# Performance work log

Measured on AMD Instinct MI355X. Metric: run time of the kernel, lower is better.

## Reference

```python
import jax, jax.numpy as jnp
import numpy as np

B, T, D = 1024, 64, 512
HID = 256          # hamiltonian_field hidden width
NH = 4             # attention heads
HD = D // NH       # head dim


def _gelu(x):
    # torch nn.GELU default = exact erf form
    return jax.nn.gelu(x, approximate=False)


def _field(z, W1, b1, W2, b2, W3, b3):
    h = _gelu(z @ W1.T + b1)
    h = _gelu(h @ W2.T + b2)
    return h @ W3.T + b3


def setup_inputs() -> dict:
    key = jax.random.key(0)
    ks = jax.random.split(key, 14)
    s = 0.02  # small-gain init like orthogonal_(gain=0.02)
    f32 = jnp.float32
    return {
        "z_init": jax.random.normal(ks[0], (B, D), f32),
        "t_steps": jnp.arange(T, dtype=f32) * 0.05,  # dt = 0.05
        "W1": jax.random.normal(ks[1], (HID, D), f32) * s,
        "b1": jnp.zeros((HID,), f32),
        "W2": jax.random.normal(ks[2], (HID, HID), f32) * s,
        "b2": jnp.zeros((HID,), f32),
        "W3": jax.random.normal(ks[3], (D, HID), f32) * s,
        "b3": jnp.zeros((D,), f32),
        "Wqkv": jax.random.normal(ks[4], (3 * D, D), f32) * (1.0 / np.sqrt(D)),
        "bqkv": jnp.zeros((3 * D,), f32),
        "Wo": jax.random.normal(ks[5], (D, D), f32) * (1.0 / np.sqrt(D)),
        "bo": jnp.zeros((D,), f32),
        "gamma": jnp.ones((D,), f32),
        "beta": jnp.zeros((D,), f32),
    }


def _forward(z_init, t_steps, W1, b1, W2, b2, W3, b3, Wqkv, bqkv, Wo, bo, gamma, beta):
    dt = t_steps[1] - t_steps[0]
    # input-adaptive scale, computed under no_grad in torch
    zn = jnp.linalg.norm(z_init, axis=-1, keepdims=True)
    zv = jnp.var(z_init, axis=-1, ddof=1, keepdims=True)  # torch.var unbiased
    scale = jax.lax.stop_gradient(jnp.clip(zn / (zv + 1e-6), 0.8, 1.2))
    z0 = z_init * scale

    f = lambda z: _field(z, W1, b1, W2, b2, W3, b3)

    def rk4_step(zt, _):
        k1 = f(zt)
        k2 = f(zt + dt * 0.5 * k1)
        k3 = f(zt + dt * 0.5 * k2)
        k4 = f(zt + dt * k3)
        z_new = zt + dt / 6.0 * (k1 + 2.0 * k2 + 2.0 * k3 + k4)
        z_new = jnp.where(jnp.isnan(z_new), 0.0, z_new)
        return z_new, z_new

    _, outs = jax.lax.scan(rk4_step, z0, None, length=T)  # [T,B,D]
    z_stack = jnp.transpose(outs, (1, 0, 2))              # [B,T,D]

    z_mean = jnp.mean(z_stack, axis=1, keepdims=True)
    z_dc = z_stack - 0.05 * (z_mean - z_init[:, None, :])

    # (torch code also computes rfft magnitudes / argmax here, but the result
    # is unused in the returned output, so it is omitted.)

    # multi-head self-attention, batch_first
    qkv = z_dc @ Wqkv.T + bqkv                            # [B,T,3D]
    q, k, v = jnp.split(qkv, 3, axis=-1)
    q = q.reshape(B, T, NH, HD)
    k = k.reshape(B, T, NH, HD)
    v = v.reshape(B, T, NH, HD)
    scores = jnp.einsum("bqhd,bkhd->bhqk", q, k) / jnp.sqrt(jnp.float32(HD))
    att = jax.nn.softmax(scores, axis=-1)
    ctx = jnp.einsum("bhqk,bkhd->bqhd", att, v).reshape(B, T, D)
    att_out = ctx @ Wo.T + bo

    # residual + LayerNorm (eps=1e-5)
    x = z_dc + att_out
    mu = jnp.mean(x, axis=-1, keepdims=True)
    var = jnp.var(x, axis=-1, keepdims=True)
    z_final = (x - mu) / jnp.sqrt(var + 1e-5) * gamma + beta
    z_final = jnp.where(jnp.isnan(z_final), 0.0, z_final)
    return z_final


def reference(z_init, t_steps, W1, b1, W2, b2, W3, b3, Wqkv, bqkv, Wo, bo, gamma, beta):
    return _forward(z_init, t_steps, W1, b1, W2, b2, W3, b3, Wqkv, bqkv, Wo, bo, gamma, beta)
```

## Files before the change

### kernel.cpp

```cpp
#include <hip/hip_runtime.h>

typedef short s16;
typedef short bf16x8 __attribute__((ext_vector_type(8)));
typedef float f32x4 __attribute__((ext_vector_type(4)));

constexpr int kB = 1024, kT = 64, kD = 512, kH = 256;
constexpr int NSEG = 14;
constexpr int kOff[NSEG] = {0, 524288, 524352, 655424, 655680, 721216, 721472,
                            852544, 853056, 1639488, 1641024, 1903168, 1903680, 1904192};
constexpr int kTotalConv = 1904704;

__device__ __forceinline__ float bs2f(s16 s) {
    return __uint_as_float(((unsigned)(unsigned short)s) << 16);
}
__device__ __forceinline__ s16 f2bs(float f) {
    unsigned u = __float_as_uint(f);
    unsigned r = (u + 0x7fffu + ((u >> 16) & 1u)) >> 16;
    return (s16)r;
}
__device__ __forceinline__ f32x4 mfma16(bf16x8 a, bf16x8 b, f32x4 c) {
    return __builtin_amdgcn_mfma_f32_16x16x32_bf16(a, b, c, 0, 0, 0);
}
__device__ __forceinline__ float gelu(float x) {
    return 0.5f * x * (1.0f + erff(x * 0.70710678118654752f));
}

__global__ void detect_kernel(const unsigned* __restrict__ ts, int* __restrict__ flag) {
    if (threadIdx.x == 0 && blockIdx.x == 0) flag[0] = (ts[0] == 0u) ? 1 : 0;
}

struct ConvArgs { const void* src[NSEG]; };

__global__ __launch_bounds__(256) void convert_kernel(ConvArgs a, s16* __restrict__ dst,
                                                      const int* __restrict__ flag) {
    const int f = flag[0];
    for (int i = blockIdx.x * 256 + threadIdx.x; i < kTotalConv; i += gridDim.x * 256) {
        int s = 0;
        #pragma unroll
        for (int j = 1; j < NSEG; ++j) if (i >= kOff[j]) s = j;
        int local = i - kOff[s];
        s16 v;
        if (f) v = f2bs(((const float*)a.src[s])[local]);
        else   v = ((const s16*)a.src[s])[local];
        dst[i] = v;
    }
}

__global__ __launch_bounds__(512, 2) void ode_kernel(
    const s16* __restrict__ zin, const s16* __restrict__ ts,
    const s16* __restrict__ W1, const s16* __restrict__ b1,
    const s16* __restrict__ W2, const s16* __restrict__ b2,
    const s16* __restrict__ W3, const s16* __restrict__ b3,
    s16* __restrict__ stage)
{
    __shared__ __align__(16) s16 sArg[16 * 520];
    __shared__ __align__(16) s16 sH1[16 * 264];
    __shared__ __align__(16) s16 sH2[16 * 264];
    __shared__ float sScale[16];

    const int tid = threadIdx.x;
    const int w = tid >> 6;
    const int lane = tid & 63;
    const int quad = lane >> 4;
    const int c = lane & 15;
    const int r0 = blockIdx.x * 16;

    const float dt  = bs2f(ts[1]) - bs2f(ts[0]);
    const float hdt = 0.5f * dt;
    const float dt6 = dt / 6.0f;

    for (int r = w; r < 16; r += 8) {
        const s16* zrow = zin + (size_t)(r0 + r) * kD;
        float sum = 0.f, ssq = 0.f;
        for (int i = 0; i < 8; ++i) {
            float v = bs2f(zrow[lane + 64 * i]);
            sum += v; ssq += v * v;
        }
        for (int m = 1; m < 64; m <<= 1) {
            sum += __shfl_xor(sum, m, 64);
            ssq += __shfl_xor(ssq, m, 64);
        }
        float zn = sqrtf(ssq);
        float mean = sum / (float)kD;
        float var = (ssq - (float)kD * mean * mean) / (float)(kD - 1);
        float sc = zn / (var + 1e-6f);
        sc = fminf(fmaxf(sc, 0.8f), 1.2f);
        if (lane == 0) sScale[r] = sc;
    }

    bf16x8 w2r[2][8];
    #pragma unroll
    for (int nt = 0; nt < 2; ++nt)
        #pragma unroll
        for (int kk = 0; kk < 8; ++kk)
            w2r[nt][kk] = *(const bf16x8*)(W2 + (size_t)(w * 32 + nt * 16 + c) * kH + kk * 32 + quad * 8);

    __syncthreads();

    const int colbase = w * 64;
    float zreg[4][4], accR[4][4];
    #pragma unroll
    for (int nt = 0; nt < 4; ++nt)
        #pragma unroll
        for (int rr = 0; rr < 4; ++rr) {
            int m = quad * 4 + rr, col = colbase + nt * 16 + c;
            zreg[nt][rr] = bs2f(zin[(size_t)(r0 + m) * kD + col]) * sScale[m];
            accR[nt][rr] = 0.f;
        }
    for (int r = w; r < 16; r += 8) {
        const s16* zrow = zin + (size_t)(r0 + r) * kD;
        float sc = sScale[r];
        s16* dst = sArg + r * 520 + lane * 8;
        #pragma unroll
        for (int j = 0; j < 8; ++j) dst[j] = f2bs(bs2f(zrow[lane * 8 + j]) * sc);
    }
    float b1v[2], b2v[2], b3v[4];
    #pragma unroll
    for (int nt = 0; nt < 2; ++nt) {
        b1v[nt] = bs2f(b1[w * 32 + nt * 16 + c]);
        b2v[nt] = bs2f(b2[w * 32 + nt * 16 + c]);
    }
    #pragma unroll
    for (int nt = 0; nt < 4; ++nt) b3v[nt] = bs2f(b3[colbase + nt * 16 + c]);

    const int w1o = (w * 32 + c) * kD + quad * 8;
    const int w3o = (w * 64 + c) * kH + quad * 8;

    __syncthreads();

    #pragma unroll 1
    for (int t = 0; t < kT; ++t) {
        #pragma unroll 1
        for (int e = 0; e < 4; ++e) {
            int ow1 = w1o, ow3 = w3o;
            asm volatile("" : "+v"(ow1), "+v"(ow3));
            const s16* W1p = W1 + ow1;
            const s16* W3p = W3 + ow3;

            f32x4 a1[2];
            a1[0] = {0.f, 0.f, 0.f, 0.f};
            a1[1] = {0.f, 0.f, 0.f, 0.f};
            #pragma unroll
            for (int kk = 0; kk < 16; ++kk) {
                bf16x8 av = *(const bf16x8*)(sArg + c * 520 + kk * 32 + quad * 8);
                bf16x8 b0 = *(const bf16x8*)(W1p + kk * 32);
                bf16x8 b1f = *(const bf16x8*)(W1p + 16 * kD + kk * 32);
                a1[0] = mfma16(av, b0, a1[0]);
                a1[1] = mfma16(av, b1f, a1[1]);
            }
            #pragma unroll
            for (int nt = 0; nt < 2; ++nt)
                #pragma unroll
                for (int rr = 0; rr < 4; ++rr)
                    sH1[(quad * 4 + rr) * 264 + w * 32 + nt * 16 + c] = f2bs(gelu(a1[nt][rr] + b1v[nt]));
            __syncthreads();

            f32x4 a2[2];
            a2[0] = {0.f, 0.f, 0.f, 0.f};
            a2[1] = {0.f, 0.f, 0.f, 0.f};
            #pragma unroll
            for (int kk = 0; kk < 8; ++kk) {
                bf16x8 av = *(const bf16x8*)(sH1 + c * 264 + kk * 32 + quad * 8);
                a2[0] = mfma16(av, w2r[0][kk], a2[0]);
                a2[1] = mfma16(av, w2r[1][kk], a2[1]);
            }
            #pragma unroll
            for (int nt = 0; nt < 2; ++nt)
                #pragma unroll
                for (int rr = 0; rr < 4; ++rr)
                    sH2[(quad * 4 + rr) * 264 + w * 32 + nt * 16 + c] = f2bs(gelu(a2[nt][rr] + b2v[nt]));
            __syncthreads();

            f32x4 a3[4];
            #pragma unroll
            for (int nt = 0; nt < 4; ++nt) a3[nt] = {0.f, 0.f, 0.f, 0.f};
            #pragma unroll
            for (int kk = 0; kk < 8; ++kk) {
                bf16x8 av = *(const bf16x8*)(sH2 + c * 264 + kk * 32 + quad * 8);
                #pragma unroll
                for (int nt = 0; nt < 4; ++nt) {
                    bf16x8 bb = *(const bf16x8*)(W3p + nt * 16 * kH + kk * 32);
                    a3[nt] = mfma16(av, bb, a3[nt]);
                }
            }
            const float wsum = (e == 0 || e == 3) ? 1.f : 2.f;
            const float cstep = (e == 2) ? dt : hdt;
            #pragma unroll
            for (int nt = 0; nt < 4; ++nt) {
                #pragma unroll
                for (int rr = 0; rr < 4; ++rr) {
                    float fv = a3[nt][rr] + b3v[nt];
                    accR[nt][rr] += wsum * fv;
                    int m = quad * 4 + rr;
                    int col = colbase + nt * 16 + c;
                    float argv;
                    if (e < 3) {
                        argv = zreg[nt][rr] + cstep * fv;
                    } else {
                        float zn2 = zreg[nt][rr] + dt6 * accR[nt][rr];
                        zn2 = (zn2 != zn2) ? 0.f : zn2;
                        zreg[nt][rr] = zn2;
                        accR[nt][rr] = 0.f;
                        argv = zn2;
                        stage[(size_t)(r0 + m) * kT * kD + (size_t)t * kD + col] = f2bs(zn2);
                    }
                    sArg[m * 520 + col] = f2bs(argv);
                }
            }
            __syncthreads();
        }
    }
}

__global__ __launch_bounds__(256) void attn_kernel(
    const s16* __restrict__ zin,
    const s16* __restrict__ Wqkv, const s16* __restrict__ bqkv,
    const s16* __restrict__ Wo, const s16* __restrict__ bo,
    const s16* __restrict__ gm, const s16* __restrict__ bt,
    const s16* __restrict__ stage, void* __restrict__ outp,
    const int* __restrict__ flag, int mode)
{
    __shared__ __align__(16) s16 sQ[64 * 136];
    __shared__ __align__(16) s16 sK[64 * 136];
    __shared__ __align__(16) s16 sVT[128 * 72];
    __shared__ __align__(16) s16 sMean[512];
    __shared__ __align__(16) s16 sZi[512];
    float* psum = (float*)sQ;

    const int tid = threadIdx.x;
    const int w = tid >> 6, lane = tid & 63, quad = lane >> 4, c = lane & 15;
    const int b = blockIdx.x;
    const int f32out = mode ? flag[0] : 0;
    const s16* zs = stage + (size_t)b * kT * kD;

    for (int i = tid; i < kD; i += 256) sZi[i] = zin[(size_t)b * kD + i];
    {
        float s[8] = {0, 0, 0, 0, 0, 0, 0, 0};
        const int phase = tid >> 6, cg = (tid & 63) * 8;
        for (int i = 0; i < 16; ++i) {
            int t = phase + 4 * i;
            bf16x8 v = *(const bf16x8*)(zs + (size_t)t * kD + cg);
            #pragma unroll
            for (int j = 0; j < 8; ++j) s[j] += bs2f(v[j]);
        }
        #pragma unroll
        for (int j = 0; j < 8; ++j) psum[phase * kD + cg + j] = s[j];
    }
    __syncthreads();
    for (int col = tid; col < kD; col += 256) {
        float m = (psum[col] + psum[kD + col] + psum[2 * kD + col] + psum[3 * kD + col]) * (1.f / 64.f);
        sMean[col] = f2bs(m);
    }
    __syncthreads();

    bf16x8 afrag[16];
    #pragma unroll
    for (int kk = 0; kk < 16; ++kk) {
        int k0 = kk * 32 + quad * 8;
        bf16x8 zv = *(const bf16x8*)(zs + (size_t)(w * 16 + c) * kD + k0);
        bf16x8 o;
        #pragma unroll
        for (int j = 0; j < 8; ++j) {
            float zd = bs2f(zv[j]) - 0.05f * (bs2f(sMean[k0 + j]) - bs2f(sZi[k0 + j]));
            o[j] = f2bs(zd);
        }
        afrag[kk] = o;
    }

    f32x4 xacc[32];
    #pragma unroll
    for (int nt = 0; nt < 32; ++nt) xacc[nt] = {0.f, 0.f, 0.f, 0.f};

    const float iscl = 0.08838834764831845f;

    for (int h = 0; h < 4; ++h) {
        __syncthreads();
        for (int mat = 0; mat < 3; ++mat) {
            f32x4 acc[8];
            #pragma unroll
            for (int nt = 0; nt < 8; ++nt) acc[nt] = {0.f, 0.f, 0.f, 0.f};
            const s16* Wbase = Wqkv + (size_t)(mat * 512 + h * 128 + c) * kD + quad * 8;
            #pragma unroll
            for (int kk = 0; kk < 16; ++kk) {
                bf16x8 a = afrag[kk];
                #pragma unroll
                for (int nt = 0; nt < 8; ++nt) {
                    bf16x8 bb = *(const bf16x8*)(Wbase + (size_t)(nt * 16) * kD + kk * 32);
                    acc[nt] = mfma16(a, bb, acc[nt]);
                }
            }
            #pragma unroll
            for (int nt = 0; nt < 8; ++nt)
                #pragma unroll
                for (int rr = 0; rr < 4; ++rr) {
                    int n = h * 128 + nt * 16 + c;
                    float v = acc[nt][rr] + bs2f(bqkv[mat * 512 + n]);
                    int trow = w * 16 + quad * 4 + rr, dcol = nt * 16 + c;
                    if (mat == 0)      sQ[trow * 136 + dcol] = f2bs(v);
                    else if (mat == 1) sK[trow * 136 + dcol] = f2bs(v);
                    else               sVT[dcol * 72 + trow] = f2bs(v);
                }
        }
        __syncthreads();

        f32x4 sfr[4];
        #pragma unroll
        for (int nt = 0; nt < 4; ++nt) sfr[nt] = {0.f, 0.f, 0.f, 0.f};
        #pragma unroll
        for (int kk = 0; kk < 4; ++kk) {
            bf16x8 a = *(const bf16x8*)(sQ + (w * 16 + c) * 136 + kk * 32 + quad * 8);
            #pragma unroll
            for (int nt = 0; nt < 4; ++nt) {
                bf16x8 bb = *(const bf16x8*)(sK + (nt * 16 + c) * 136 + kk * 32 + quad * 8);
                sfr[nt] = mfma16(a, bb, sfr[nt]);
            }
        }
        #pragma unroll
        for (int rr = 0; rr < 4; ++rr) {
            float v[4];
            #pragma unroll
            for (int nt = 0; nt < 4; ++nt) v[nt] = sfr[nt][rr] * iscl;
            float mx = fmaxf(fmaxf(v[0], v[1]), fmaxf(v[2], v[3]));
            for (int m = 1; m < 16; m <<= 1) mx = fmaxf(mx, __shfl_xor(mx, m, 64));
            float sm = 0.f;
            #pragma unroll
            for (int nt = 0; nt < 4; ++nt) { v[nt] = __expf(v[nt] - mx); sm += v[nt]; }
            for (int m = 1; m < 16; m <<= 1) sm += __shfl_xor(sm, m, 64);
            float inv = 1.0f / sm;
            #pragma unroll
            for (int nt = 0; nt < 4; ++nt)
                sQ[(w * 16 + quad * 4 + rr) * 136 + nt * 16 + c] = f2bs(v[nt] * inv);
        }
        f32x4 o[8];
        #pragma unroll
        for (int nt = 0; nt < 8; ++nt) o[nt] = {0.f, 0.f, 0.f, 0.f};
        #pragma unroll
        for (int kk = 0; kk < 2; ++kk) {
            bf16x8 a = *(const bf16x8*)(sQ + (w * 16 + c) * 136 + kk * 32 + quad * 8);
            #pragma unroll
            for (int nt = 0; nt < 8; ++nt) {
                bf16x8 bb = *(const bf16x8*)(sVT + (nt * 16 + c) * 72 + kk * 32 + quad * 8);
                o[nt] = mfma16(a, bb, o[nt]);
            }
        }
        #pragma unroll
        for (int nt = 0; nt < 8; ++nt)
            #pragma unroll
            for (int rr = 0; rr < 4; ++rr)
                sQ[(w * 16 + quad * 4 + rr) * 136 + nt * 16 + c] = f2bs(o[nt][rr]);
        #pragma unroll
        for (int kk = 0; kk < 4; ++kk) {
            bf16x8 a = *(const bf16x8*)(sQ + (w * 16 + c) * 136 + kk * 32 + quad * 8);
            #pragma unroll
            for (int nt = 0; nt < 32; ++nt) {
                bf16x8 bb = *(const bf16x8*)(Wo + (size_t)(nt * 16 + c) * kD + h * 128 + kk * 32 + quad * 8);
                xacc[nt] = mfma16(a, bb, xacc[nt]);
            }
        }
    }

    float sum[4] = {0, 0, 0, 0}, ssq[4] = {0, 0, 0, 0};
    #pragma unroll
    for (int nt = 0; nt < 32; ++nt)
        #pragma unroll
        for (int rr = 0; rr < 4; ++rr) {
            int trow = w * 16 + quad * 4 + rr;
            int col = nt * 16 + c;
            float zd = bs2f(zs[(size_t)trow * kD + col]) - 0.05f * (bs2f(sMean[col]) - bs2f(sZi[col]));
            float x = xacc[nt][rr] + bs2f(bo[col]) + zd;
            xacc[nt][rr] = x;
            sum[rr] += x; ssq[rr] += x * x;
        }
    float mu[4], rstd[4];
    #pragma unroll
    for (int rr = 0; rr < 4; ++rr) {
        float s = sum[rr], q = ssq[rr];
        for (int m = 1; m < 16; m <<= 1) { s += __shfl_xor(s, m, 64); q += __shfl_xor(q, m, 64); }
        float mm = s / (float)kD;
        float var = q / (float)kD - mm * mm;
        mu[rr] = mm;
        rstd[rr] = rsqrtf(var + 1e-5f);
    }
    #pragma unroll
    for (int nt = 0; nt < 32; ++nt)
        #pragma unroll
        for (int rr = 0; rr < 4; ++rr) {
            int trow = w * 16 + quad * 4 + rr;
            int col = nt * 16 + c;
            float v = (xacc[nt][rr] - mu[rr]) * rstd[rr] * bs2f(gm[col]) + bs2f(bt[col]);
            v = (v != v) ? 0.f : v;
            size_t idx = ((size_t)b * kT + trow) * kD + col;
            if (f32out) ((float*)outp)[idx] = v;
            else        ((s16*)outp)[idx] = f2bs(v);
        }
}

extern "C" void kernel_launch(void* const* d_in, const int* in_sizes, int n_in,
                              void* d_out, int out_size, void* d_ws, size_t ws_size,
                              hipStream_t stream) {
    (void)in_sizes; (void)n_in; (void)out_size;
    const size_t kStageElems = (size_t)kB * kT * kD;
    const size_t kNeed = 16 + (size_t)kTotalConv * 2 + kStageElems * 2;

    const s16* p[NSEG];
    s16* stage;
    void* outp = d_out;
    const int* flag = nullptr;
    int mode = 0;

    if (ws_size >= kNeed) {
        int* flg = (int*)d_ws;
        s16* conv = (s16*)((char*)d_ws + 16);
        stage = (s16*)((char*)d_ws + 16 + (size_t)kTotalConv * 2);
        detect_kernel<<<dim3(1), dim3(64), 0, stream>>>((const unsigned*)d_in[1], flg);
        ConvArgs ca;
        for (int i = 0; i < NSEG; ++i) ca.src[i] = d_in[i];
        convert_kernel<<<dim3(512), dim3(256), 0, stream>>>(ca, conv, flg);
        for (int i = 0; i < NSEG; ++i) p[i] = conv + kOff[i];
        flag = flg;
        mode = 1;
    } else {
        for (int i = 0; i < NSEG; ++i) p[i] = (const s16*)d_in[i];
        stage = (s16*)d_out;
    }

    ode_kernel<<<dim3(64), dim3(512), 0, stream>>>(
        p[0], p[1], p[2], p[3], p[4], p[5], p[6], p[7], stage);
    attn_kernel<<<dim3(kB), dim3(256), 0, stream>>>(
        p[0], p[8], p[9], p[10], p[11], p[12], p[13], stage, outp, flag, mode);
}
```

Before: 6.275 ms.

## Batch weight loads with inline-asm dwordx4 and prefetch W3 during layer two

Replaces compiler-scheduled W1/W3 global loads inside the RK4 field evaluation with explicit inline-asm global_load_dwordx4 batches of 16 registers, each followed by a single vmcnt(0) wait. The W3 loads for the first half of layer 3 are issued before the layer-2 MFMAs and the barrier, so their latency can overlap that work. The goal is to hide global or L2 load latency that previously stalled the MFMA chains. In exchange the kernel holds more live VGPRs for the staged weights, and the blanket vmcnt(0) waits may over-serialize.

```diff
diff --git a/kernel.cpp b/kernel.cpp
--- a/kernel.cpp
+++ b/kernel.cpp
@@ -24,6 +24,11 @@
 __device__ __forceinline__ float gelu(float x) {
     return 0.5f * x * (1.0f + erff(x * 0.70710678118654752f));
 }
+
+#define GLD(dst, ptr, OFF) \
+    asm volatile("global_load_dwordx4 %0, %1, off offset:" #OFF : "=v"(dst) : "v"(ptr))
+#define VMWAIT0 do { asm volatile("s_waitcnt vmcnt(0)" ::: "memory"); \
+                     __builtin_amdgcn_sched_barrier(0); } while (0)
 
 __global__ void detect_kernel(const unsigned* __restrict__ ts, int* __restrict__ flag) {
     if (threadIdx.x == 0 && blockIdx.x == 0) flag[0] = (ts[0] == 0u) ? 1 : 0;
@@ -87,14 +92,6 @@
         sc = fminf(fmaxf(sc, 0.8f), 1.2f);
         if (lane == 0) sScale[r] = sc;
     }
-
-    bf16x8 w2r[2][8];
-    #pragma unroll
-    for (int nt = 0; nt < 2; ++nt)
-        #pragma unroll
-        for (int kk = 0; kk < 8; ++kk)
-            w2r[nt][kk] = *(const bf16x8*)(W2 + (size_t)(w * 32 + nt * 16 + c) * kH + kk * 32 + quad * 8);
-
     __syncthreads();
 
     const int colbase = w * 64;
@@ -123,8 +120,25 @@
     #pragma unroll
     for (int nt = 0; nt < 4; ++nt) b3v[nt] = bs2f(b3[colbase + nt * 16 + c]);
 
-    const int w1o = (w * 32 + c) * kD + quad * 8;
-    const int w3o = (w * 64 + c) * kH + quad * 8;
+    const s16* w1p0 = W1 + (size_t)(w * 32 + c) * kD + quad * 8;
+    const s16* w1p1 = w1p0 + 16 * kD;
+    const s16* w2p0 = W2 + (size_t)(w * 32 + c) * kH + quad * 8;
+    const s16* w2p1 = w2p0 + 16 * kH;
+    const s16* w3p0 = W3 + (size_t)(w * 64 + c) * kH + quad * 8;
+    const s16* w3p1 = w3p0 + 16 * kH;
+    const s16* w3p2 = w3p0 + 32 * kH;
+    const s16* w3p3 = w3p0 + 48 * kH;
+
+    bf16x8 w2r[16];
+    GLD(w2r[0],  w2p0, 0);   GLD(w2r[1],  w2p1, 0);
+    GLD(w2r[2],  w2p0, 64);  GLD(w2r[3],  w2p1, 64);
+    GLD(w2r[4],  w2p0, 128); GLD(w2r[5],  w2p1, 128);
+    GLD(w2r[6],  w2p0, 192); GLD(w2r[7],  w2p1, 192);
+    GLD(w2r[8],  w2p0, 256); GLD(w2r[9],  w2p1, 256);
+    GLD(w2r[10], w2p0, 320); GLD(w2r[11], w2p1, 320);
+    GLD(w2r[12], w2p0, 384); GLD(w2r[13], w2p1, 384);
+    GLD(w2r[14], w2p0, 448); GLD(w2r[15], w2p1, 448);
+    VMWAIT0;
 
     __syncthreads();
 
@@ -132,57 +146,105 @@
     for (int t = 0; t < kT; ++t) {
         #pragma unroll 1
         for (int e = 0; e < 4; ++e) {
-            int ow1 = w1o, ow3 = w3o;
-            asm volatile("" : "+v"(ow1), "+v"(ow3));
-            const s16* W1p = W1 + ow1;
-            const s16* W3p = W3 + ow3;
-
-            f32x4 a1[2];
-            a1[0] = {0.f, 0.f, 0.f, 0.f};
-            a1[1] = {0.f, 0.f, 0.f, 0.f};
-            #pragma unroll
-            for (int kk = 0; kk < 16; ++kk) {
-                bf16x8 av = *(const bf16x8*)(sArg + c * 520 + kk * 32 + quad * 8);
-                bf16x8 b0 = *(const bf16x8*)(W1p + kk * 32);
-                bf16x8 b1f = *(const bf16x8*)(W1p + 16 * kD + kk * 32);
-                a1[0] = mfma16(av, b0, a1[0]);
-                a1[1] = mfma16(av, b1f, a1[1]);
-            }
-            #pragma unroll
-            for (int nt = 0; nt < 2; ++nt)
-                #pragma unroll
-                for (int rr = 0; rr < 4; ++rr)
-                    sH1[(quad * 4 + rr) * 264 + w * 32 + nt * 16 + c] = f2bs(gelu(a1[nt][rr] + b1v[nt]));
+            f32x4 a1n0 = {0.f, 0.f, 0.f, 0.f}, a1n1 = {0.f, 0.f, 0.f, 0.f};
+            {
+                bf16x8 wf[16];
+                GLD(wf[0],  w1p0, 0);   GLD(wf[1],  w1p1, 0);
+                GLD(wf[2],  w1p0, 64);  GLD(wf[3],  w1p1, 64);
+                GLD(wf[4],  w1p0, 128); GLD(wf[5],  w1p1, 128);
+                GLD(wf[6],  w1p0, 192); GLD(wf[7],  w1p1, 192);
+                GLD(wf[8],  w1p0, 256); GLD(wf[9],  w1p1, 256);
+                GLD(wf[10], w1p0, 320); GLD(wf[11], w1p1, 320);
+                GLD(wf[12], w1p0, 384); GLD(wf[13], w1p1, 384);
+                GLD(wf[14], w1p0, 448); GLD(wf[15], w1p1, 448);
+                VMWAIT0;
+                #pragma unroll
+                for (int kk = 0; kk < 8; ++kk) {
+                    bf16x8 av = *(const bf16x8*)(sArg + c * 520 + kk * 32 + quad * 8);
+                    a1n0 = mfma16(av, wf[kk * 2 + 0], a1n0);
+                    a1n1 = mfma16(av, wf[kk * 2 + 1], a1n1);
+                }
+                GLD(wf[0],  w1p0, 512); GLD(wf[1],  w1p1, 512);
+                GLD(wf[2],  w1p0, 576); GLD(wf[3],  w1p1, 576);
+                GLD(wf[4],  w1p0, 640); GLD(wf[5],  w1p1, 640);
+                GLD(wf[6],  w1p0, 704); GLD(wf[7],  w1p1, 704);
+                GLD(wf[8],  w1p0, 768); GLD(wf[9],  w1p1, 768);
+                GLD(wf[10], w1p0, 832); GLD(wf[11], w1p1, 832);
+                GLD(wf[12], w1p0, 896); GLD(wf[13], w1p1, 896);
+                GLD(wf[14], w1p0, 960); GLD(wf[15], w1p1, 960);
+                VMWAIT0;
+                #pragma unroll
+                for (int kk = 0; kk < 8; ++kk) {
+                    bf16x8 av = *(const bf16x8*)(sArg + c * 520 + (8 + kk) * 32 + quad * 8);
+                    a1n0 = mfma16(av, wf[kk * 2 + 0], a1n0);
+                    a1n1 = mfma16(av, wf[kk * 2 + 1], a1n1);
+                }
+            }
+            sH1[(quad * 4 + 0) * 264 + w * 32 + 0 * 16 + c] = f2bs(gelu(a1n0[0] + b1v[0]));
+            sH1[(quad * 4 + 1) * 264 + w * 32 + 0 * 16 + c] = f2bs(gelu(a1n0[1] + b1v[0]));
+            sH1[(quad * 4 + 2) * 264 + w * 32 + 0 * 16 + c] = f2bs(gelu(a1n0[2] + b1v[0]));
+            sH1[(quad * 4 + 3) * 264 + w * 32 + 0 * 16 + c] = f2bs(gelu(a1n0[3] + b1v[0]));
+            sH1[(quad * 4 + 0) * 264 + w * 32 + 1 * 16 + c] = f2bs(gelu(a1n1[0] + b1v[1]));
+            sH1[(quad * 4 + 1) * 264 + w * 32 + 1 * 16 + c] = f2bs(gelu(a1n1[1] + b1v[1]));
+            sH1[(quad * 4 + 2) * 264 + w * 32 + 1 * 16 + c] = f2bs(gelu(a1n1[2] + b1v[1]));
+            sH1[(quad * 4 + 3) * 264 + w * 32 + 1 * 16 + c] = f2bs(gelu(a1n1[3] + b1v[1]));
             __syncthreads();
 
-            f32x4 a2[2];
-            a2[0] = {0.f, 0.f, 0.f, 0.f};
-            a2[1] = {0.f, 0.f, 0.f, 0.f};
+            bf16x8 w3x[16];
+            GLD(w3x[0],  w3p0, 0);   GLD(w3x[1],  w3p1, 0);
+            GLD(w3x[2],  w3p2, 0);   GLD(w3x[3],  w3p3, 0);
+            GLD(w3x[4],  w3p0, 64);  GLD(w3x[5],  w3p1, 64);
+            GLD(w3x[6],  w3p2, 64);  GLD(w3x[7],  w3p3, 64);
+            GLD(w3x[8],  w3p0, 128); GLD(w3x[9],  w3p1, 128);
+            GLD(w3x[10], w3p2, 128); GLD(w3x[11], w3p3, 128);
+            GLD(w3x[12], w3p0, 192); GLD(w3x[13], w3p1, 192);
+            GLD(w3x[14], w3p2, 192); GLD(w3x[15], w3p3, 192);
+
+            f32x4 a2n0 = {0.f, 0.f, 0.f, 0.f}, a2n1 = {0.f, 0.f, 0.f, 0.f};
             #pragma unroll
             for (int kk = 0; kk < 8; ++kk) {
                 bf16x8 av = *(const bf16x8*)(sH1 + c * 264 + kk * 32 + quad * 8);
-                a2[0] = mfma16(av, w2r[0][kk], a2[0]);
-                a2[1] = mfma16(av, w2r[1][kk], a2[1]);
-            }
-            #pragma unroll
-            for (int nt = 0; nt < 2; ++nt)
-                #pragma unroll
-                for (int rr = 0; rr < 4; ++rr)
-                    sH2[(quad * 4 + rr) * 264 + w * 32 + nt * 16 + c] = f2bs(gelu(a2[nt][rr] + b2v[nt]));
+                a2n0 = mfma16(av, w2r[kk * 2 + 0], a2n0);
+                a2n1 = mfma16(av, w2r[kk * 2 + 1], a2n1);
+            }
+            sH2[(quad * 4 + 0) * 264 + w * 32 + 0 * 16 + c] = f2bs(gelu(a2n0[0] + b2v[0]));
+            sH2[(quad * 4 + 1) * 264 + w * 32 + 0 * 16 + c] = f2bs(gelu(a2n0[1] + b2v[0]));
+            sH2[(quad * 4 + 2) * 264 + w * 32 + 0 * 16 + c] = f2bs(gelu(a2n0[2] + b2v[0]));
+            sH2[(quad * 4 + 3) * 264 + w * 32 + 0 * 16 + c] = f2bs(gelu(a2n0[3] + b2v[0]));
+            sH2[(quad * 4 + 0) * 264 + w * 32 + 1 * 16 + c] = f2bs(gelu(a2n1[0] + b2v[1]));
+            sH2[(quad * 4 + 1) * 264 + w * 32 + 1 * 16 + c] = f2bs(gelu(a2n1[1] + b2v[1]));
+            sH2[(quad * 4 + 2) * 264 + w * 32 + 1 * 16 + c] = f2bs(gelu(a2n1[2] + b2v[1]));
+            sH2[(quad * 4 + 3) * 264 + w * 32 + 1 * 16 + c] = f2bs(gelu(a2n1[3] + b2v[1]));
             __syncthreads();
 
+            VMWAIT0;
             f32x4 a3[4];
             #pragma unroll
             for (int nt = 0; nt < 4; ++nt) a3[nt] = {0.f, 0.f, 0.f, 0.f};
             #pragma unroll
-            for (int kk = 0; kk < 8; ++kk) {
+            for (int kk = 0; kk < 4; ++kk) {
                 bf16x8 av = *(const bf16x8*)(sH2 + c * 264 + kk * 32 + quad * 8);
                 #pragma unroll
-                for (int nt = 0; nt < 4; ++nt) {
-                    bf16x8 bb = *(const bf16x8*)(W3p + nt * 16 * kH + kk * 32);
-                    a3[nt] = mfma16(av, bb, a3[nt]);
-                }
-            }
+                for (int nt = 0; nt < 4; ++nt)
+                    a3[nt] = mfma16(av, w3x[kk * 4 + nt], a3[nt]);
+            }
+            GLD(w3x[0],  w3p0, 256); GLD(w3x[1],  w3p1, 256);
+            GLD(w3x[2],  w3p2, 256); GLD(w3x[3],  w3p3, 256);
+            GLD(w3x[4],  w3p0, 320); GLD(w3x[5],  w3p1, 320);
+            GLD(w3x[6],  w3p2, 320); GLD(w3x[7],  w3p3, 320);
+            GLD(w3x[8],  w3p0, 384); GLD(w3x[9],  w3p1, 384);
+            GLD(w3x[10], w3p2, 384); GLD(w3x[11], w3p3, 384);
+            GLD(w3x[12], w3p0, 448); GLD(w3x[13], w3p1, 448);
+            GLD(w3x[14], w3p2, 448); GLD(w3x[15], w3p3, 448);
+            VMWAIT0;
+            #pragma unroll
+            for (int kk = 0; kk < 4; ++kk) {
+                bf16x8 av = *(const bf16x8*)(sH2 + c * 264 + (4 + kk) * 32 + quad * 8);
+                #pragma unroll
+                for (int nt = 0; nt < 4; ++nt)
+                    a3[nt] = mfma16(av, w3x[kk * 4 + nt], a3[nt]);
+            }
+
             const float wsum = (e == 0 || e == 3) ? 1.f : 2.f;
             const float cstep = (e == 2) ? dt : hdt;
             #pragma unroll
```

Measured after the change: 6.122 ms. 2.4% less time.

## Split ODE field work over 16 waves with hand-pipelined weight loads

Applied to the files above, without the earlier changes.

Doubles the ODE block to 1024 threads (16 waves), so each wave owns half as many output columns per layer. W2 is no longer held in registers and is reloaded every stage. W1, W2 and W3 fragments are now fetched with inline-asm dwordx4 loads issued ahead of use, with staged vmcnt waits so global latency overlaps the MFMA chains. Barriers become a raw lgkmcnt wait plus s_barrier. The aim is to hide the latency of the serial RK4 chain with more waves and explicit prefetch, at the cost of more weight traffic from L2 and fragile hand-counted waits.

```diff
diff --git a/kernel.cpp b/kernel.cpp
--- a/kernel.cpp
+++ b/kernel.cpp
@@ -24,6 +24,15 @@
 __device__ __forceinline__ float gelu(float x) {
     return 0.5f * x * (1.0f + erff(x * 0.70710678118654752f));
 }
+
+#define GLD(dst, ptr, OFF) \
+    asm volatile("global_load_dwordx4 %0, %1, off offset:" #OFF : "=v"(dst) : "v"(ptr))
+#define VMWAIT(N) do { asm volatile("s_waitcnt vmcnt(" #N ")" ::: "memory"); \
+                       __builtin_amdgcn_sched_barrier(0); } while (0)
+#define LDSBAR do { asm volatile("s_waitcnt lgkmcnt(0)" ::: "memory"); \
+                    __builtin_amdgcn_s_barrier(); \
+                    asm volatile("" ::: "memory"); \
+                    __builtin_amdgcn_sched_barrier(0); } while (0)
 
 __global__ void detect_kernel(const unsigned* __restrict__ ts, int* __restrict__ flag) {
     if (threadIdx.x == 0 && blockIdx.x == 0) flag[0] = (ts[0] == 0u) ? 1 : 0;
@@ -46,7 +55,7 @@
     }
 }
 
-__global__ __launch_bounds__(512, 2) void ode_kernel(
+__global__ __launch_bounds__(1024) void ode_kernel(
     const s16* __restrict__ zin, const s16* __restrict__ ts,
     const s16* __restrict__ W1, const s16* __restrict__ b1,
     const s16* __restrict__ W2, const s16* __restrict__ b2,
@@ -69,8 +78,8 @@
     const float hdt = 0.5f * dt;
     const float dt6 = dt / 6.0f;
 
-    for (int r = w; r < 16; r += 8) {
-        const s16* zrow = zin + (size_t)(r0 + r) * kD;
+    {
+        const s16* zrow = zin + (size_t)(r0 + w) * kD;
         float sum = 0.f, ssq = 0.f;
         for (int i = 0; i < 8; ++i) {
             float v = bs2f(zrow[lane + 64 * i]);
@@ -85,46 +94,37 @@
         float var = (ssq - (float)kD * mean * mean) / (float)(kD - 1);
         float sc = zn / (var + 1e-6f);
         sc = fminf(fmaxf(sc, 0.8f), 1.2f);
-        if (lane == 0) sScale[r] = sc;
-    }
-
-    bf16x8 w2r[2][8];
+        if (lane == 0) sScale[w] = sc;
+    }
+    __syncthreads();
+
+    const int colbase = w * 32;
+    float zreg[2][4], accR[2][4];
     #pragma unroll
     for (int nt = 0; nt < 2; ++nt)
-        #pragma unroll
-        for (int kk = 0; kk < 8; ++kk)
-            w2r[nt][kk] = *(const bf16x8*)(W2 + (size_t)(w * 32 + nt * 16 + c) * kH + kk * 32 + quad * 8);
-
-    __syncthreads();
-
-    const int colbase = w * 64;
-    float zreg[4][4], accR[4][4];
-    #pragma unroll
-    for (int nt = 0; nt < 4; ++nt)
         #pragma unroll
         for (int rr = 0; rr < 4; ++rr) {
             int m = quad * 4 + rr, col = colbase + nt * 16 + c;
             zreg[nt][rr] = bs2f(zin[(size_t)(r0 + m) * kD + col]) * sScale[m];
             accR[nt][rr] = 0.f;
         }
-    for (int r = w; r < 16; r += 8) {
-        const s16* zrow = zin + (size_t)(r0 + r) * kD;
-        float sc = sScale[r];
-        s16* dst = sArg + r * 520 + lane * 8;
+    {
+        const s16* zrow = zin + (size_t)(r0 + w) * kD;
+        float sc = sScale[w];
+        s16* dst = sArg + w * 520 + lane * 8;
         #pragma unroll
         for (int j = 0; j < 8; ++j) dst[j] = f2bs(bs2f(zrow[lane * 8 + j]) * sc);
     }
-    float b1v[2], b2v[2], b3v[4];
-    #pragma unroll
-    for (int nt = 0; nt < 2; ++nt) {
-        b1v[nt] = bs2f(b1[w * 32 + nt * 16 + c]);
-        b2v[nt] = bs2f(b2[w * 32 + nt * 16 + c]);
-    }
-    #pragma unroll
-    for (int nt = 0; nt < 4; ++nt) b3v[nt] = bs2f(b3[colbase + nt * 16 + c]);
-
-    const int w1o = (w * 32 + c) * kD + quad * 8;
-    const int w3o = (w * 64 + c) * kH + quad * 8;
+    const float b1v = bs2f(b1[w * 16 + c]);
+    const float b2v = bs2f(b2[w * 16 + c]);
+    float b3v[2];
+    b3v[0] = bs2f(b3[colbase + c]);
+    b3v[1] = bs2f(b3[colbase + 16 + c]);
+
+    const s16* w1p  = W1 + (size_t)(w * 16 + c) * kD + quad * 8;
+    const s16* w2p  = W2 + (size_t)(w * 16 + c) * kH + quad * 8;
+    const s16* w3p0 = W3 + (size_t)(w * 32 + c) * kH + quad * 8;
+    const s16* w3p1 = w3p0 + 16 * kH;
 
     __syncthreads();
 
@@ -132,61 +132,94 @@
     for (int t = 0; t < kT; ++t) {
         #pragma unroll 1
         for (int e = 0; e < 4; ++e) {
-            int ow1 = w1o, ow3 = w3o;
-            asm volatile("" : "+v"(ow1), "+v"(ow3));
-            const s16* W1p = W1 + ow1;
-            const s16* W3p = W3 + ow3;
-
-            f32x4 a1[2];
-            a1[0] = {0.f, 0.f, 0.f, 0.f};
-            a1[1] = {0.f, 0.f, 0.f, 0.f};
-            #pragma unroll
-            for (int kk = 0; kk < 16; ++kk) {
+            bf16x8 f1a[8], f1b[8], f2w[8];
+            GLD(f1a[0], w1p, 0);   GLD(f1a[1], w1p, 64);
+            GLD(f1a[2], w1p, 128); GLD(f1a[3], w1p, 192);
+            GLD(f1a[4], w1p, 256); GLD(f1a[5], w1p, 320);
+            GLD(f1a[6], w1p, 384); GLD(f1a[7], w1p, 448);
+            GLD(f1b[0], w1p, 512); GLD(f1b[1], w1p, 576);
+            GLD(f1b[2], w1p, 640); GLD(f1b[3], w1p, 704);
+            GLD(f1b[4], w1p, 768); GLD(f1b[5], w1p, 832);
+            GLD(f1b[6], w1p, 896); GLD(f1b[7], w1p, 960);
+            VMWAIT(8);
+            f32x4 a1 = {0.f, 0.f, 0.f, 0.f};
+            #pragma unroll
+            for (int kk = 0; kk < 8; ++kk) {
                 bf16x8 av = *(const bf16x8*)(sArg + c * 520 + kk * 32 + quad * 8);
-                bf16x8 b0 = *(const bf16x8*)(W1p + kk * 32);
-                bf16x8 b1f = *(const bf16x8*)(W1p + 16 * kD + kk * 32);
-                a1[0] = mfma16(av, b0, a1[0]);
-                a1[1] = mfma16(av, b1f, a1[1]);
-            }
-            #pragma unroll
-            for (int nt = 0; nt < 2; ++nt)
-                #pragma unroll
-                for (int rr = 0; rr < 4; ++rr)
-                    sH1[(quad * 4 + rr) * 264 + w * 32 + nt * 16 + c] = f2bs(gelu(a1[nt][rr] + b1v[nt]));
-            __syncthreads();
-
-            f32x4 a2[2];
-            a2[0] = {0.f, 0.f, 0.f, 0.f};
-            a2[1] = {0.f, 0.f, 0.f, 0.f};
+                a1 = mfma16(av, f1a[kk], a1);
+            }
+            GLD(f2w[0], w2p, 0);   GLD(f2w[1], w2p, 64);
+            GLD(f2w[2], w2p, 128); GLD(f2w[3], w2p, 192);
+            GLD(f2w[4], w2p, 256); GLD(f2w[5], w2p, 320);
+            GLD(f2w[6], w2p, 384); GLD(f2w[7], w2p, 448);
+            VMWAIT(8);
+            #pragma unroll
+            for (int kk = 0; kk < 8; ++kk) {
+                bf16x8 av = *(const bf16x8*)(sArg + c * 520 + (8 + kk) * 32 + quad * 8);
+                a1 = mfma16(av, f1b[kk], a1);
+            }
+            #pragma unroll
+            for (int rr = 0; rr < 4; ++rr)
+                sH1[(quad * 4 + rr) * 264 + w * 16 + c] = f2bs(gelu(a1[rr] + b1v));
+            LDSBAR;
+
+            bf16x8 f3a[4], f3b[4], f3c[4], f3d[4];
+            GLD(f3a[0], w3p0, 0);   GLD(f3a[1], w3p1, 0);
+            GLD(f3a[2], w3p0, 64);  GLD(f3a[3], w3p1, 64);
+            GLD(f3b[0], w3p0, 128); GLD(f3b[1], w3p1, 128);
+            GLD(f3b[2], w3p0, 192); GLD(f3b[3], w3p1, 192);
+            VMWAIT(8);
+            f32x4 a2 = {0.f, 0.f, 0.f, 0.f};
             #pragma unroll
             for (int kk = 0; kk < 8; ++kk) {
                 bf16x8 av = *(const bf16x8*)(sH1 + c * 264 + kk * 32 + quad * 8);
-                a2[0] = mfma16(av, w2r[0][kk], a2[0]);
-                a2[1] = mfma16(av, w2r[1][kk], a2[1]);
-            }
-            #pragma unroll
-            for (int nt = 0; nt < 2; ++nt)
-                #pragma unroll
-                for (int rr = 0; rr < 4; ++rr)
-                    sH2[(quad * 4 + rr) * 264 + w * 32 + nt * 16 + c] = f2bs(gelu(a2[nt][rr] + b2v[nt]));
-            __syncthreads();
-
-            f32x4 a3[4];
-            #pragma unroll
-            for (int nt = 0; nt < 4; ++nt) a3[nt] = {0.f, 0.f, 0.f, 0.f};
-            #pragma unroll
-            for (int kk = 0; kk < 8; ++kk) {
+                a2 = mfma16(av, f2w[kk], a2);
+            }
+            GLD(f3c[0], w3p0, 256); GLD(f3c[1], w3p1, 256);
+            GLD(f3c[2], w3p0, 320); GLD(f3c[3], w3p1, 320);
+            GLD(f3d[0], w3p0, 384); GLD(f3d[1], w3p1, 384);
+            GLD(f3d[2], w3p0, 448); GLD(f3d[3], w3p1, 448);
+            #pragma unroll
+            for (int rr = 0; rr < 4; ++rr)
+                sH2[(quad * 4 + rr) * 264 + w * 16 + c] = f2bs(gelu(a2[rr] + b2v));
+            LDSBAR;
+
+            f32x4 a3[2];
+            a3[0] = {0.f, 0.f, 0.f, 0.f};
+            a3[1] = {0.f, 0.f, 0.f, 0.f};
+            VMWAIT(12);
+            #pragma unroll
+            for (int kk = 0; kk < 2; ++kk) {
                 bf16x8 av = *(const bf16x8*)(sH2 + c * 264 + kk * 32 + quad * 8);
-                #pragma unroll
-                for (int nt = 0; nt < 4; ++nt) {
-                    bf16x8 bb = *(const bf16x8*)(W3p + nt * 16 * kH + kk * 32);
-                    a3[nt] = mfma16(av, bb, a3[nt]);
-                }
-            }
+                a3[0] = mfma16(av, f3a[kk * 2 + 0], a3[0]);
+                a3[1] = mfma16(av, f3a[kk * 2 + 1], a3[1]);
+            }
+            VMWAIT(8);
+            #pragma unroll
+            for (int kk = 2; kk < 4; ++kk) {
+                bf16x8 av = *(const bf16x8*)(sH2 + c * 264 + kk * 32 + quad * 8);
+                a3[0] = mfma16(av, f3b[(kk - 2) * 2 + 0], a3[0]);
+                a3[1] = mfma16(av, f3b[(kk - 2) * 2 + 1], a3[1]);
+            }
+            VMWAIT(4);
+            #pragma unroll
+            for (int kk = 4; kk < 6; ++kk) {
+                bf16x8 av = *(const bf16x8*)(sH2 + c * 264 + kk * 32 + quad * 8);
+                a3[0] = mfma16(av, f3c[(kk - 4) * 2 + 0], a3[0]);
+                a3[1] = mfma16(av, f3c[(kk - 4) * 2 + 1], a3[1]);
+            }
+            VMWAIT(0);
+            #pragma unroll
+            for (int kk = 6; kk < 8; ++kk) {
+                bf16x8 av = *(const bf16x8*)(sH2 + c * 264 + kk * 32 + quad * 8);
+                a3[0] = mfma16(av, f3d[(kk - 6) * 2 + 0], a3[0]);
+                a3[1] = mfma16(av, f3d[(kk - 6) * 2 + 1], a3[1]);
+            }
+
             const float wsum = (e == 0 || e == 3) ? 1.f : 2.f;
             const float cstep = (e == 2) ? dt : hdt;
             #pragma unroll
-            for (int nt = 0; nt < 4; ++nt) {
+            for (int nt = 0; nt < 2; ++nt) {
                 #pragma unroll
                 for (int rr = 0; rr < 4; ++rr) {
                     float fv = a3[nt][rr] + b3v[nt];
@@ -207,7 +240,7 @@
                     sArg[m * 520 + col] = f2bs(argv);
                 }
             }
-            __syncthreads();
+            LDSBAR;
         }
     }
 }
@@ -424,7 +457,7 @@
         stage = (s16*)d_out;
     }
 
-    ode_kernel<<<dim3(64), dim3(512), 0, stream>>>(
+    ode_kernel<<<dim3(64), dim3(1024), 0, stream>>>(
         p[0], p[1], p[2], p[3], p[4], p[5], p[6], p[7], stage);
     attn_kernel<<<dim3(kB), dim3(256), 0, stream>>>(
         p[0], p[8], p[9], p[10], p[11], p[12], p[13], stage, outp, flag, mode);
```

New measurement: 6.710 ms. 1.07x slower.

## Split ODE MLP work across 16 waves per block instead of 8

Applied to the files above, without the earlier changes.

The ODE kernel now launches 1024 threads (16 waves) per block, so each wave computes 16 hidden columns and 32 output columns instead of 32 and 64. This doubles the waves available to hide latency in the serial RK4 loop and halves per-wave MFMA chains. W2 is no longer cached in registers and is read from global memory every stage. The extra waves also make each block barrier more costly.

```diff
diff --git a/kernel.cpp b/kernel.cpp
--- a/kernel.cpp
+++ b/kernel.cpp
@@ -46,7 +46,7 @@
     }
 }
 
-__global__ __launch_bounds__(512, 2) void ode_kernel(
+__global__ __launch_bounds__(1024) void ode_kernel(
     const s16* __restrict__ zin, const s16* __restrict__ ts,
     const s16* __restrict__ W1, const s16* __restrict__ b1,
     const s16* __restrict__ W2, const s16* __restrict__ b2,
@@ -69,8 +69,8 @@
     const float hdt = 0.5f * dt;
     const float dt6 = dt / 6.0f;
 
-    for (int r = w; r < 16; r += 8) {
-        const s16* zrow = zin + (size_t)(r0 + r) * kD;
+    {
+        const s16* zrow = zin + (size_t)(r0 + w) * kD;
         float sum = 0.f, ssq = 0.f;
         for (int i = 0; i < 8; ++i) {
             float v = bs2f(zrow[lane + 64 * i]);
@@ -85,111 +85,82 @@
         float var = (ssq - (float)kD * mean * mean) / (float)(kD - 1);
         float sc = zn / (var + 1e-6f);
         sc = fminf(fmaxf(sc, 0.8f), 1.2f);
-        if (lane == 0) sScale[r] = sc;
-    }
-
-    bf16x8 w2r[2][8];
+        if (lane == 0) sScale[w] = sc;
+    }
+    __syncthreads();
+
+    const int colbase = w * 32;
+    float zreg[2][4], accR[2][4];
     #pragma unroll
     for (int nt = 0; nt < 2; ++nt)
-        #pragma unroll
-        for (int kk = 0; kk < 8; ++kk)
-            w2r[nt][kk] = *(const bf16x8*)(W2 + (size_t)(w * 32 + nt * 16 + c) * kH + kk * 32 + quad * 8);
-
-    __syncthreads();
-
-    const int colbase = w * 64;
-    float zreg[4][4], accR[4][4];
-    #pragma unroll
-    for (int nt = 0; nt < 4; ++nt)
         #pragma unroll
         for (int rr = 0; rr < 4; ++rr) {
             int m = quad * 4 + rr, col = colbase + nt * 16 + c;
             zreg[nt][rr] = bs2f(zin[(size_t)(r0 + m) * kD + col]) * sScale[m];
             accR[nt][rr] = 0.f;
         }
-    for (int r = w; r < 16; r += 8) {
-        const s16* zrow = zin + (size_t)(r0 + r) * kD;
-        float sc = sScale[r];
-        s16* dst = sArg + r * 520 + lane * 8;
+    {
+        const s16* zrow = zin + (size_t)(r0 + w) * kD;
+        float sc = sScale[w];
+        s16* dst = sArg + w * 520 + lane * 8;
         #pragma unroll
         for (int j = 0; j < 8; ++j) dst[j] = f2bs(bs2f(zrow[lane * 8 + j]) * sc);
     }
-    float b1v[2], b2v[2], b3v[4];
-    #pragma unroll
-    for (int nt = 0; nt < 2; ++nt) {
-        b1v[nt] = bs2f(b1[w * 32 + nt * 16 + c]);
-        b2v[nt] = bs2f(b2[w * 32 + nt * 16 + c]);
-    }
-    #pragma unroll
-    for (int nt = 0; nt < 4; ++nt) b3v[nt] = bs2f(b3[colbase + nt * 16 + c]);
-
-    const int w1o = (w * 32 + c) * kD + quad * 8;
-    const int w3o = (w * 64 + c) * kH + quad * 8;
-
+    const float b1v = bs2f(b1[w * 16 + c]);
+    const float b2v = bs2f(b2[w * 16 + c]);
+    const float b3v0 = bs2f(b3[colbase + c]);
+    const float b3v1 = bs2f(b3[colbase + 16 + c]);
     __syncthreads();
 
     #pragma unroll 1
     for (int t = 0; t < kT; ++t) {
         #pragma unroll 1
         for (int e = 0; e < 4; ++e) {
-            int ow1 = w1o, ow3 = w3o;
-            asm volatile("" : "+v"(ow1), "+v"(ow3));
-            const s16* W1p = W1 + ow1;
-            const s16* W3p = W3 + ow3;
-
-            f32x4 a1[2];
-            a1[0] = {0.f, 0.f, 0.f, 0.f};
-            a1[1] = {0.f, 0.f, 0.f, 0.f};
-            #pragma unroll
-            for (int kk = 0; kk < 16; ++kk) {
-                bf16x8 av = *(const bf16x8*)(sArg + c * 520 + kk * 32 + quad * 8);
-                bf16x8 b0 = *(const bf16x8*)(W1p + kk * 32);
-                bf16x8 b1f = *(const bf16x8*)(W1p + 16 * kD + kk * 32);
-                a1[0] = mfma16(av, b0, a1[0]);
-                a1[1] = mfma16(av, b1f, a1[1]);
-            }
-            #pragma unroll
-            for (int nt = 0; nt < 2; ++nt)
-                #pragma unroll
-                for (int rr = 0; rr < 4; ++rr)
-                    sH1[(quad * 4 + rr) * 264 + w * 32 + nt * 16 + c] = f2bs(gelu(a1[nt][rr] + b1v[nt]));
+            f32x4 a1 = {0.f, 0.f, 0.f, 0.f};
+            {
+                const bf16x8* Ap = (const bf16x8*)(sArg + c * 520 + quad * 8);
+                const bf16x8* Bp = (const bf16x8*)(W1 + (size_t)(w * 16 + c) * kD + quad * 8);
+                #pragma unroll
+                for (int kk = 0; kk < 16; ++kk)
+                    a1 = mfma16(Ap[kk * 4], Bp[kk * 4], a1);
+            }
+            #pragma unroll
+            for (int rr = 0; rr < 4; ++rr)
+                sH1[(quad * 4 + rr) * 264 + w * 16 + c] = f2bs(gelu(a1[rr] + b1v));
             __syncthreads();
 
-            f32x4 a2[2];
-            a2[0] = {0.f, 0.f, 0.f, 0.f};
-            a2[1] = {0.f, 0.f, 0.f, 0.f};
-            #pragma unroll
-            for (int kk = 0; kk < 8; ++kk) {
-                bf16x8 av = *(const bf16x8*)(sH1 + c * 264 + kk * 32 + quad * 8);
-                a2[0] = mfma16(av, w2r[0][kk], a2[0]);
-                a2[1] = mfma16(av, w2r[1][kk], a2[1]);
-            }
-            #pragma unroll
-            for (int nt = 0; nt < 2; ++nt)
-                #pragma unroll
-                for (int rr = 0; rr < 4; ++rr)
-                    sH2[(quad * 4 + rr) * 264 + w * 32 + nt * 16 + c] = f2bs(gelu(a2[nt][rr] + b2v[nt]));
+            f32x4 a2 = {0.f, 0.f, 0.f, 0.f};
+            {
+                const bf16x8* Ap = (const bf16x8*)(sH1 + c * 264 + quad * 8);
+                const bf16x8* Bp = (const bf16x8*)(W2 + (size_t)(w * 16 + c) * kH + quad * 8);
+                #pragma unroll
+                for (int kk = 0; kk < 8; ++kk)
+                    a2 = mfma16(Ap[kk * 4], Bp[kk * 4], a2);
+            }
+            #pragma unroll
+            for (int rr = 0; rr < 4; ++rr)
+                sH2[(quad * 4 + rr) * 264 + w * 16 + c] = f2bs(gelu(a2[rr] + b2v));
             __syncthreads();
 
-            f32x4 a3[4];
-            #pragma unroll
-            for (int nt = 0; nt < 4; ++nt) a3[nt] = {0.f, 0.f, 0.f, 0.f};
-            #pragma unroll
-            for (int kk = 0; kk < 8; ++kk) {
-                bf16x8 av = *(const bf16x8*)(sH2 + c * 264 + kk * 32 + quad * 8);
-                #pragma unroll
-                for (int nt = 0; nt < 4; ++nt) {
-                    bf16x8 bb = *(const bf16x8*)(W3p + nt * 16 * kH + kk * 32);
-                    a3[nt] = mfma16(av, bb, a3[nt]);
+            f32x4 a3n0 = {0.f, 0.f, 0.f, 0.f}, a3n1 = {0.f, 0.f, 0.f, 0.f};
+            {
+                const bf16x8* Ap = (const bf16x8*)(sH2 + c * 264 + quad * 8);
+                const bf16x8* B0 = (const bf16x8*)(W3 + (size_t)(colbase + c) * kH + quad * 8);
+                const bf16x8* B1 = (const bf16x8*)(W3 + (size_t)(colbase + 16 + c) * kH + quad * 8);
+                #pragma unroll
+                for (int kk = 0; kk < 8; ++kk) {
+                    bf16x8 av = Ap[kk * 4];
+                    a3n0 = mfma16(av, B0[kk * 4], a3n0);
+                    a3n1 = mfma16(av, B1[kk * 4], a3n1);
                 }
             }
             const float wsum = (e == 0 || e == 3) ? 1.f : 2.f;
             const float cstep = (e == 2) ? dt : hdt;
             #pragma unroll
-            for (int nt = 0; nt < 4; ++nt) {
+            for (int nt = 0; nt < 2; ++nt) {
                 #pragma unroll
                 for (int rr = 0; rr < 4; ++rr) {
-                    float fv = a3[nt][rr] + b3v[nt];
+                    float fv = ((nt == 0) ? a3n0[rr] : a3n1[rr]) + ((nt == 0) ? b3v0 : b3v1);
                     accR[nt][rr] += wsum * fv;
                     int m = quad * 4 + rr;
                     int col = colbase + nt * 16 + c;
@@ -424,7 +395,7 @@
         stage = (s16*)d_out;
     }
 
-    ode_kernel<<<dim3(64), dim3(512), 0, stream>>>(
+    ode_kernel<<<dim3(64), dim3(1024), 0, stream>>>(
         p[0], p[1], p[2], p[3], p[4], p[5], p[6], p[7], stage);
     attn_kernel<<<dim3(kB), dim3(256), 0, stream>>>(
         p[0], p[8], p[9], p[10], p[11], p[12], p[13], stage, outp, flag, mode);
```

New measurement: 5.118 ms. 1.23x faster.
